# Optimization experiments

Hardware: AMD Instinct MI355X
Metric: run time of the kernel (lower is better)

The kernel has to match this reference:

```python
import jax, jax.numpy as jnp
import numpy as np

N, D = 128, 512  # batch, hypercube dim (in_features == n_2d_layers == out_features)

def setup_inputs() -> dict:
    key = jax.random.key(0)
    k1, k2, k3 = jax.random.split(key, 3)
    bound = 1.0 / np.sqrt(D)
    x = jax.random.normal(k1, (N, D, D), dtype=jnp.float32)
    # kaiming_uniform_(a=sqrt(5)) on (in, layers, out) ~ U(-1/sqrt(fan_in), 1/sqrt(fan_in)) scale
    w = jax.random.uniform(k2, (D, D, D), dtype=jnp.float32, minval=-bound, maxval=bound)
    b = jax.random.uniform(k3, (D, D), dtype=jnp.float32, minval=-bound, maxval=bound)
    return {"x": x, "w": w, "b": b}

def reference(x, w, b):
    # Original: (x.expand((L, *x.shape)).movedim(0,-2) * w).sum(-1) + b
    # which reduces to out[n,i,j] = sum_k x[n,i,k] * w[i,j,k] + b[i,j]
    # (w axes: (in_features, n_2d_layers, out_features), all equal D)
    return jnp.einsum('nik,ijk->nij', x, w) + b
```

## Files before the change

kernel.cpp:

```cpp
#include <hip/hip_runtime.h>


#define Dd 512
#define CHUNK 16
#define NCHUNK 32

typedef __attribute__((ext_vector_type(8))) short bf16x8;
typedef __attribute__((ext_vector_type(4))) short bf16x4;
typedef __attribute__((ext_vector_type(4))) float f32x4;

__device__ __forceinline__ short f2bf(float f) {
    unsigned u = __builtin_bit_cast(unsigned, f);
    u += 0x7FFFu + ((u >> 16) & 1u);
    return (short)(u >> 16);
}

__device__ __forceinline__ void glds16(const float* g, float* l) {
    __builtin_amdgcn_global_load_lds(
        (const __attribute__((address_space(1))) void*)g,
        (__attribute__((address_space(3))) void*)l, 16, 0, 0);
}

__global__ __launch_bounds__(512, 4)
void linear3d_kernel(const float* __restrict__ x,
                     const float* __restrict__ w,
                     const float* __restrict__ b,
                     float* __restrict__ out) {
    const int i    = blockIdx.x;
    const int tid  = threadIdx.x;
    const int lane = tid & 63;
    const int wid  = tid >> 6;

    __shared__ float f32s[CHUNK * Dd];
    __shared__ short b16[2][CHUNK * Dd];
    __shared__ float ldsb[Dd];

    const float* xi = x + (size_t)i * Dd;
    const float* wi = w + (size_t)i * Dd * Dd;

    ldsb[tid] = b[i * Dd + tid];

    #pragma unroll
    for (int q = 0; q < 4; ++q)
        glds16(wi + (size_t)(wid * 256 + q * 64 + lane) * 4,
               &f32s[(wid * 256 + q * 64) * 4]);

    short* xstage = &b16[0][0];
    bf16x8 xf[16];
    #pragma unroll 4
    for (int r = 0; r < 4; ++r) {
        __syncthreads();
        #pragma unroll
        for (int p = 0; p < 8; ++p) {
            int idx4 = tid + p * 512;
            int row  = idx4 >> 7, c4 = idx4 & 127;
            float4 v = *(const float4*)(xi + (size_t)(r * 32 + row) * (Dd * Dd) + c4 * 4);
            bf16x4 h = { f2bf(v.x), f2bf(v.y), f2bf(v.z), f2bf(v.w) };
            int byte = row * 1024 + c4 * 8;
            byte ^= (row & 7) << 4;
            *(bf16x4*)((char*)xstage + byte) = h;
        }
        __syncthreads();
        if ((wid >> 1) == r) {
            int row = (wid & 1) * 16 + (lane & 15);
            #pragma unroll
            for (int s = 0; s < 16; ++s) {
                int byte = row * 1024 + s * 64 + (lane >> 4) * 16;
                byte ^= (row & 7) << 4;
                xf[s] = *(const bf16x8*)((const char*)xstage + byte);
            }
        }
    }
    __syncthreads();

    #pragma unroll
    for (int p = 0; p < 4; ++p) {
        int idx4 = tid + p * 512;
        int row = idx4 >> 7, cu = idx4 & 127;
        float4 v = *(const float4*)(f32s + idx4 * 4);
        bf16x4 h = { f2bf(v.x), f2bf(v.y), f2bf(v.z), f2bf(v.w) };
        int byte = row * 1024 + cu * 8;
        byte ^= (row & 7) << 4;
        *(bf16x4*)((char*)&b16[0][0] + byte) = h;
    }
    asm volatile("s_waitcnt lgkmcnt(0)" ::: "memory");
    __builtin_amdgcn_s_barrier();

    #pragma unroll
    for (int q = 0; q < 4; ++q)
        glds16(wi + (size_t)(CHUNK * Dd) + (size_t)(wid * 256 + q * 64 + lane) * 4,
               &f32s[(wid * 256 + q * 64) * 4]);

    const int row16 = lane & 15;
    const int nb = wid * 16;
    float* outbase = out + (size_t)i * Dd;

    for (int c = 0; c < NCHUNK; ++c) {
        const char* buf = (const char*)&b16[c & 1][0];
        f32x4 acc = {0.f, 0.f, 0.f, 0.f};
        #pragma unroll
        for (int s = 0; s < 16; ++s) {
            int byte = row16 * 1024 + s * 64 + (lane >> 4) * 16;
            byte ^= (row16 & 7) << 4;
            bf16x8 wf = *(const bf16x8*)(buf + byte);
            acc = __builtin_amdgcn_mfma_f32_16x16x32_bf16(xf[s], wf, acc, 0, 0, 0);
        }
        float bias = ldsb[c * 16 + row16];
        #pragma unroll
        for (int r = 0; r < 4; ++r) {
            int n = nb + (lane >> 4) * 4 + r;
            outbase[(size_t)n * (Dd * Dd) + c * CHUNK + row16] = acc[r] + bias;
        }

        if (c + 1 < NCHUNK) {
            asm volatile("s_waitcnt lgkmcnt(0) vmcnt(4)" ::: "memory");
            __builtin_amdgcn_s_barrier();

            char* dstb = (char*)&b16[(c + 1) & 1][0];
            #pragma unroll
            for (int p = 0; p < 4; ++p) {
                int idx4 = tid + p * 512;
                int row = idx4 >> 7, cu = idx4 & 127;
                float4 v = *(const float4*)(f32s + idx4 * 4);
                bf16x4 h = { f2bf(v.x), f2bf(v.y), f2bf(v.z), f2bf(v.w) };
                int byte = row * 1024 + cu * 8;
                byte ^= (row & 7) << 4;
                *(bf16x4*)(dstb + byte) = h;
            }
            asm volatile("s_waitcnt lgkmcnt(0)" ::: "memory");
            __builtin_amdgcn_s_barrier();

            if (c + 2 < NCHUNK) {
                const float* src = wi + (size_t)(c + 2) * (CHUNK * Dd);
                #pragma unroll
                for (int q = 0; q < 4; ++q)
                    glds16(src + (size_t)(wid * 256 + q * 64 + lane) * 4,
                           &f32s[(wid * 256 + q * 64) * 4]);
            }
        }
    }
}

extern "C" void kernel_launch(void* const* d_in, const int* in_sizes, int n_in,
                              void* d_out, int out_size, void* d_ws, size_t ws_size,
                              hipStream_t stream) {
    const float* x = (const float*)d_in[0];
    const float* w = (const float*)d_in[1];
    const float* b = (const float*)d_in[2];
    float* out = (float*)d_out;
    linear3d_kernel<<<dim3(Dd), dim3(512), 0, stream>>>(x, w, b, out);
}
```

Before: 184.8 us.

## Deepen weight prefetch to two fp32 staging buffers with single bf16 tile

Restructures the per-layer weight pipeline: two fp32 LDS staging buffers are kept in flight via global_load_lds, three chunks ahead, and a single bf16 buffer is converted per chunk. Each wave converts only its own rows, and loads for the next chunk are issued right after the staged values are read into registers. Fine-grained vmcnt waits and sched barriers replace the coarser wait. The MFMA loop is split into two independent accumulators and bias is read straight from global memory. The aim is to hide HBM weight-load latency behind compute. The cost is hand-tuned vmcnt counts that must stay exactly right, and x staging now runs in 8 rounds instead of 4.

```diff
diff --git a/kernel.cpp b/kernel.cpp
--- a/kernel.cpp
+++ b/kernel.cpp
@@ -2,8 +2,7 @@
 
 
 #define Dd 512
-#define CHUNK 16
-#define NCHUNK 32
+#define DD (512 * 512)
 
 typedef __attribute__((ext_vector_type(8))) short bf16x8;
 typedef __attribute__((ext_vector_type(4))) short bf16x4;
@@ -30,115 +29,121 @@
     const int tid  = threadIdx.x;
     const int lane = tid & 63;
     const int wid  = tid >> 6;
+    const int row16 = lane & 15;
+    const int cg    = lane >> 4;
 
-    __shared__ float f32s[CHUNK * Dd];
-    __shared__ short b16[2][CHUNK * Dd];
-    __shared__ float ldsb[Dd];
+    __shared__ float f32r[2][8192];
+    __shared__ short b16s[8192];
 
     const float* xi = x + (size_t)i * Dd;
-    const float* wi = w + (size_t)i * Dd * Dd;
-
-    ldsb[tid] = b[i * Dd + tid];
+    const float* wi = w + (size_t)i * DD;
 
     #pragma unroll
-    for (int q = 0; q < 4; ++q)
-        glds16(wi + (size_t)(wid * 256 + q * 64 + lane) * 4,
-               &f32s[(wid * 256 + q * 64) * 4]);
+    for (int q = 0; q < 4; ++q) { int t = wid * 4 + q;
+        glds16(wi + t * 256 + lane * 4, &f32r[0][t * 256]); }
+    #pragma unroll
+    for (int q = 0; q < 4; ++q) { int t = wid * 4 + q;
+        glds16(wi + 8192 + t * 256 + lane * 4, &f32r[1][t * 256]); }
 
-    short* xstage = &b16[0][0];
     bf16x8 xf[16];
-    #pragma unroll 4
-    for (int r = 0; r < 4; ++r) {
+    for (int r = 0; r < 8; ++r) {
         __syncthreads();
         #pragma unroll
-        for (int p = 0; p < 8; ++p) {
+        for (int p = 0; p < 4; ++p) {
             int idx4 = tid + p * 512;
-            int row  = idx4 >> 7, c4 = idx4 & 127;
-            float4 v = *(const float4*)(xi + (size_t)(r * 32 + row) * (Dd * Dd) + c4 * 4);
+            int row = idx4 >> 7, c4 = idx4 & 127;
+            float4 v = *(const float4*)(xi + (size_t)(r * 16 + row) * DD + c4 * 4);
             bf16x4 h = { f2bf(v.x), f2bf(v.y), f2bf(v.z), f2bf(v.w) };
-            int byte = row * 1024 + c4 * 8;
-            byte ^= (row & 7) << 4;
-            *(bf16x4*)((char*)xstage + byte) = h;
+            int byte = (row * 1024 + c4 * 8) ^ ((row & 7) << 4);
+            *(bf16x4*)((char*)b16s + byte) = h;
         }
         __syncthreads();
-        if ((wid >> 1) == r) {
-            int row = (wid & 1) * 16 + (lane & 15);
+        if (wid == r) {
             #pragma unroll
             for (int s = 0; s < 16; ++s) {
-                int byte = row * 1024 + s * 64 + (lane >> 4) * 16;
-                byte ^= (row & 7) << 4;
-                xf[s] = *(const bf16x8*)((const char*)xstage + byte);
+                int byte = (row16 * 1024 + s * 64 + cg * 16) ^ ((row16 & 7) << 4);
+                xf[s] = *(const bf16x8*)((const char*)b16s + byte);
             }
         }
     }
     __syncthreads();
 
-    #pragma unroll
-    for (int p = 0; p < 4; ++p) {
-        int idx4 = tid + p * 512;
-        int row = idx4 >> 7, cu = idx4 & 127;
-        float4 v = *(const float4*)(f32s + idx4 * 4);
-        bf16x4 h = { f2bf(v.x), f2bf(v.y), f2bf(v.z), f2bf(v.w) };
-        int byte = row * 1024 + cu * 8;
-        byte ^= (row & 7) << 4;
-        *(bf16x4*)((char*)&b16[0][0] + byte) = h;
+#define CVTW(V, q) do {                                                        \
+    int row_  = 2 * wid + ((q) >> 1);                                          \
+    int byte_ = (row_ * 1024 + ((q) & 1) * 512 + lane * 8) ^ ((row_ & 7) << 4);\
+    bf16x4 h_ = { f2bf(V.x), f2bf(V.y), f2bf(V.z), f2bf(V.w) };                \
+    *(bf16x4*)((char*)b16s + byte_) = h_;                                      \
+} while (0)
+
+    {
+        asm volatile("s_waitcnt vmcnt(5)" ::: "memory");
+        __builtin_amdgcn_sched_barrier(0);
+        float4 v0 = *(const float4*)(&f32r[0][wid * 1024 +   0 + lane * 4]);
+        float4 v1 = *(const float4*)(&f32r[0][wid * 1024 + 256 + lane * 4]);
+        float4 v2 = *(const float4*)(&f32r[0][wid * 1024 + 512 + lane * 4]);
+        float4 v3 = *(const float4*)(&f32r[0][wid * 1024 + 768 + lane * 4]);
+        asm volatile("s_waitcnt lgkmcnt(0)" ::: "memory");
+        __builtin_amdgcn_sched_barrier(0);
+        #pragma unroll
+        for (int q = 0; q < 4; ++q) { int t = wid * 4 + q;
+            glds16(wi + 2 * 8192 + t * 256 + lane * 4, &f32r[0][t * 256]); }
+        CVTW(v0, 0); CVTW(v1, 1); CVTW(v2, 2); CVTW(v3, 3);
     }
+    float bias = b[i * Dd + row16];
     asm volatile("s_waitcnt lgkmcnt(0)" ::: "memory");
     __builtin_amdgcn_s_barrier();
 
-    #pragma unroll
-    for (int q = 0; q < 4; ++q)
-        glds16(wi + (size_t)(CHUNK * Dd) + (size_t)(wid * 256 + q * 64 + lane) * 4,
-               &f32s[(wid * 256 + q * 64) * 4]);
+#define CHUNK_BODY(c, VMSTR, DO_GLDS, DO_CONV) do {                            \
+    f32x4 accA = {0.f, 0.f, 0.f, 0.f}, accB = {0.f, 0.f, 0.f, 0.f};           \
+    _Pragma("unroll")                                                          \
+    for (int s = 0; s < 16; s += 2) {                                          \
+        int byA = (row16 * 1024 + s * 64 + cg * 16) ^ ((row16 & 7) << 4);      \
+        int byB = (row16 * 1024 + (s + 1) * 64 + cg * 16) ^ ((row16 & 7) << 4);\
+        bf16x8 wfA = *(const bf16x8*)((const char*)b16s + byA);                \
+        bf16x8 wfB = *(const bf16x8*)((const char*)b16s + byB);                \
+        accA = __builtin_amdgcn_mfma_f32_16x16x32_bf16(xf[s], wfA, accA, 0, 0, 0);     \
+        accB = __builtin_amdgcn_mfma_f32_16x16x32_bf16(xf[s + 1], wfB, accB, 0, 0, 0); \
+    }                                                                          \
+    { int j = (c) * 16 + row16;                                                \
+      _Pragma("unroll")                                                        \
+      for (int r_ = 0; r_ < 4; ++r_) {                                         \
+          int n_ = wid * 16 + cg * 4 + r_;                                     \
+          out[(size_t)i * Dd + (size_t)n_ * DD + j] = accA[r_] + accB[r_] + bias; \
+      } }                                                                      \
+    asm volatile("s_waitcnt lgkmcnt(0)" ::: "memory");                         \
+    __builtin_amdgcn_s_barrier();                                              \
+    if (DO_CONV) {                                                             \
+        const float* fb = &f32r[((c) + 1) & 1][0];                             \
+        asm volatile("s_waitcnt " VMSTR ::: "memory");                         \
+        __builtin_amdgcn_sched_barrier(0);                                     \
+        float4 v0 = *(const float4*)(fb + wid * 1024 +   0 + lane * 4);        \
+        float4 v1 = *(const float4*)(fb + wid * 1024 + 256 + lane * 4);        \
+        float4 v2 = *(const float4*)(fb + wid * 1024 + 512 + lane * 4);        \
+        float4 v3 = *(const float4*)(fb + wid * 1024 + 768 + lane * 4);        \
+        asm volatile("s_waitcnt lgkmcnt(0)" ::: "memory");                     \
+        __builtin_amdgcn_sched_barrier(0);                                     \
+        if (DO_GLDS) {                                                         \
+            const float* gs = wi + (size_t)((c) + 3) * 8192;                   \
+            float* lb = &f32r[((c) + 1) & 1][0];                               \
+            _Pragma("unroll")                                                  \
+            for (int q = 0; q < 4; ++q) { int t = wid * 4 + q;                 \
+                glds16(gs + t * 256 + lane * 4, lb + t * 256); }               \
+        }                                                                      \
+        bias = b[i * Dd + ((c) + 1) * 16 + row16];                             \
+        CVTW(v0, 0); CVTW(v1, 1); CVTW(v2, 2); CVTW(v3, 3);                    \
+        asm volatile("s_waitcnt lgkmcnt(0)" ::: "memory");                     \
+        __builtin_amdgcn_s_barrier();                                          \
+    }                                                                          \
+} while (0)
 
-    const int row16 = lane & 15;
-    const int nb = wid * 16;
-    float* outbase = out + (size_t)i * Dd;
+    CHUNK_BODY(0, "vmcnt(9)", true, true);
+    for (int c = 1; c <= 29; ++c)
+        CHUNK_BODY(c, "vmcnt(14)", (c + 3 < 32), true);
+    CHUNK_BODY(30, "vmcnt(10)", false, true);
+    CHUNK_BODY(31, "vmcnt(0)", false, false);
 
-    for (int c = 0; c < NCHUNK; ++c) {
-        const char* buf = (const char*)&b16[c & 1][0];
-        f32x4 acc = {0.f, 0.f, 0.f, 0.f};
-        #pragma unroll
-        for (int s = 0; s < 16; ++s) {
-            int byte = row16 * 1024 + s * 64 + (lane >> 4) * 16;
-            byte ^= (row16 & 7) << 4;
-            bf16x8 wf = *(const bf16x8*)(buf + byte);
-            acc = __builtin_amdgcn_mfma_f32_16x16x32_bf16(xf[s], wf, acc, 0, 0, 0);
-        }
-        float bias = ldsb[c * 16 + row16];
-        #pragma unroll
-        for (int r = 0; r < 4; ++r) {
-            int n = nb + (lane >> 4) * 4 + r;
-            outbase[(size_t)n * (Dd * Dd) + c * CHUNK + row16] = acc[r] + bias;
-        }
-
-        if (c + 1 < NCHUNK) {
-            asm volatile("s_waitcnt lgkmcnt(0) vmcnt(4)" ::: "memory");
-            __builtin_amdgcn_s_barrier();
-
-            char* dstb = (char*)&b16[(c + 1) & 1][0];
-            #pragma unroll
-            for (int p = 0; p < 4; ++p) {
-                int idx4 = tid + p * 512;
-                int row = idx4 >> 7, cu = idx4 & 127;
-                float4 v = *(const float4*)(f32s + idx4 * 4);
-                bf16x4 h = { f2bf(v.x), f2bf(v.y), f2bf(v.z), f2bf(v.w) };
-                int byte = row * 1024 + cu * 8;
-                byte ^= (row & 7) << 4;
-                *(bf16x4*)(dstb + byte) = h;
-            }
-            asm volatile("s_waitcnt lgkmcnt(0)" ::: "memory");
-            __builtin_amdgcn_s_barrier();
-
-            if (c + 2 < NCHUNK) {
-                const float* src = wi + (size_t)(c + 2) * (CHUNK * Dd);
-                #pragma unroll
-                for (int q = 0; q < 4; ++q)
-                    glds16(src + (size_t)(wid * 256 + q * 64 + lane) * 4,
-                           &f32s[(wid * 256 + q * 64) * 4]);
-            }
-        }
-    }
+#undef CHUNK_BODY
+#undef CVTW
 }
 
 extern "C" void kernel_launch(void* const* d_in, const int* in_sizes, int n_in,
```

After: 205.6 us. 11.2% more time.
